# Kernel optimization log

Hardware: AMD Instinct MI355X
Metric: run time of the kernel (lower is better)

## Reference

```python
import jax, jax.numpy as jnp
import numpy as np

N_NODES = 70839  # num_user + num_item from config
N_EDGES = 2_000_000
EMB_DIM = 64
EPS = 1e-12  # torch F.normalize default eps


def setup_inputs() -> dict:
    key = jax.random.key(0)
    k1, k2, k3, k4 = jax.random.split(key, 4)
    ego_embedding = jax.random.normal(k1, (N_NODES, EMB_DIM), dtype=jnp.float32)
    edge_weight = jax.random.uniform(k2, (N_EDGES,), dtype=jnp.float32)
    edge_src = jax.random.randint(k3, (N_EDGES,), 0, N_NODES, dtype=jnp.int32)
    edge_dst = jax.random.randint(k4, (N_EDGES,), 0, N_NODES, dtype=jnp.int32)
    return {
        "ego_embedding": ego_embedding,
        "edge_weight": edge_weight,
        "edge_src": edge_src,
        "edge_dst": edge_dst,
    }


def reference(ego_embedding, edge_weight, edge_src, edge_dst):
    # message: m_e = h[src_e] * w_e   (u_mul_e)
    m = ego_embedding[edge_src] * edge_weight[:, None]          # [E, D]
    # reduce: h_v = sum_{e: dst_e = v} m_e   (fn.sum)
    h = jax.ops.segment_sum(m, edge_dst, num_segments=N_NODES)  # [N, D]
    # F.normalize(h, dim=1, p=2): x / max(||x||_2, eps)
    norm = jnp.linalg.norm(h, axis=1, keepdims=True)
    return h / jnp.maximum(norm, EPS)
```

## Files before the change

kernel.cpp:

```cpp
#include <hip/hip_runtime.h>
#include <hip/hip_fp16.h>

#define EMB_D 64
#define SB 1024
#define SPAN 128
#define MAXG 1024
#define NCHUNK2 512
#define CHMAX 4096
#define TILE 4096
#define CAST_BLOCKS 256


__device__ __forceinline__ float h15_to_float(unsigned int bits) {
    return __half2float(__ushort_as_half((unsigned short)bits));
}

__global__ void a1_cast_hist(const float2* __restrict__ embin,
                             __half2* __restrict__ emb16, int n2,
                             const int* __restrict__ dst,
                             int* __restrict__ cntT,
                             int E, int G, int chunk) {
    if (blockIdx.x < CAST_BLOCKS) {
        int i = blockIdx.x * blockDim.x + threadIdx.x;
        int st = CAST_BLOCKS * blockDim.x;
        for (; i < n2; i += st)
            emb16[i] = __float22half2_rn(embin[i]);
    } else {
        __shared__ int bins[MAXG];
        int hb = blockIdx.x - CAST_BLOCKS;
        for (int g = threadIdx.x; g < G; g += blockDim.x) bins[g] = 0;
        __syncthreads();
        int beg = hb * chunk;
        int end = min(beg + chunk, E);
        for (int i = beg + threadIdx.x; i < end; i += blockDim.x)
            atomicAdd(&bins[dst[i] >> 7], 1);
        __syncthreads();
        for (int g = threadIdx.x; g < G; g += blockDim.x)
            cntT[g * NCHUNK2 + hb] = bins[g];
    }
}

__global__ void scan_reduceB(const int* __restrict__ counts,
                             int* __restrict__ partial, int M) {
    __shared__ int wsum[16];
    const int tid = threadIdx.x, lane = tid & 63, wid = tid >> 6;
    int i = blockIdx.x * SB + tid;
    int v = (i < M) ? counts[i] : 0;
    #pragma unroll
    for (int off = 32; off > 0; off >>= 1)
        v += __shfl_xor(v, off, 64);
    if (lane == 0) wsum[wid] = v;
    __syncthreads();
    if (tid == 0) {
        int s = 0;
        #pragma unroll
        for (int k = 0; k < 16; ++k) s += wsum[k];
        partial[blockIdx.x] = s;
    }
}

__global__ void scan_partials(const int* __restrict__ partial,
                              int* __restrict__ blockoff,
                              int* __restrict__ offsets, int numB, int M) {
    __shared__ int wsum[16];
    __shared__ int wpre[16];
    __shared__ int carry;
    const int tid = threadIdx.x, lane = tid & 63, wid = tid >> 6;
    if (tid == 0) carry = 0;
    const int nPass = (numB + SB - 1) / SB;
    for (int p = 0; p < nPass; ++p) {
        __syncthreads();
        int base = carry;
        int idx = p * SB + tid;
        int v = (idx < numB) ? partial[idx] : 0;
        int x = v;
        #pragma unroll
        for (int off = 1; off < 64; off <<= 1) {
            int t = __shfl_up(x, off, 64);
            if (lane >= off) x += t;
        }
        if (lane == 63) wsum[wid] = x;
        __syncthreads();
        if (wid == 0) {
            int s = (lane < 16) ? wsum[lane] : 0;
            #pragma unroll
            for (int off = 1; off < 16; off <<= 1) {
                int t = __shfl_up(s, off, 64);
                if (lane >= off) s += t;
            }
            if (lane < 16) wpre[lane] = s;
        }
        __syncthreads();
        int excl = base + ((wid > 0) ? wpre[wid - 1] : 0) + (x - v);
        if (idx < numB) blockoff[idx] = excl;
        __syncthreads();
        if (tid == 0) carry = base + wpre[15];
    }
    __syncthreads();
    if (tid == 0) offsets[M] = carry;
}

__global__ void scan_applyB(const int* __restrict__ counts,
                            const int* __restrict__ blockoff,
                            int* __restrict__ offsets, int M) {
    __shared__ int wsum[16];
    __shared__ int wpre[16];
    const int tid = threadIdx.x, lane = tid & 63, wid = tid >> 6;
    int i = blockIdx.x * SB + tid;
    int v = (i < M) ? counts[i] : 0;
    int x = v;
    #pragma unroll
    for (int off = 1; off < 64; off <<= 1) {
        int t = __shfl_up(x, off, 64);
        if (lane >= off) x += t;
    }
    if (lane == 63) wsum[wid] = x;
    __syncthreads();
    if (wid == 0) {
        int s = (lane < 16) ? wsum[lane] : 0;
        #pragma unroll
        for (int off = 1; off < 16; off <<= 1) {
            int t = __shfl_up(s, off, 64);
            if (lane >= off) s += t;
        }
        if (lane < 16) wpre[lane] = s;
    }
    __syncthreads();
    int excl = blockoff[blockIdx.x] + ((wid > 0) ? wpre[wid - 1] : 0) + (x - v);
    if (i < M) offsets[i] = excl;
}

__global__ __launch_bounds__(512) void partition_sort(
        const int* __restrict__ src,
        const int* __restrict__ dst,
        const float* __restrict__ w,
        const int* __restrict__ cntT,
        const int* __restrict__ scanT,
        uint2* __restrict__ stream8,
        int E, int G, int chunk) {
    __shared__ uint2 recs[CHMAX];
    __shared__ int cur[MAXG];
    __shared__ int delta[MAXG];
    __shared__ int wtot[8];

    const int tid = threadIdx.x, lane = tid & 63, wv = tid >> 6;
    const int b = blockIdx.x;
    const int beg = b * chunk;
    const int end = min(beg + chunk, E);
    const int n = end - beg;

    const int K = (G + 511) >> 9;
    int vals[2];
    int acc = 0;
    #pragma unroll
    for (int k = 0; k < 2; ++k) {
        int g = tid * K + k;
        int c = (k < K && g < G) ? cntT[g * NCHUNK2 + b] : 0;
        vals[k] = c;
        acc += c;
    }
    int x = acc;
    #pragma unroll
    for (int off = 1; off < 64; off <<= 1) {
        int t = __shfl_up(x, off, 64);
        if (lane >= off) x += t;
    }
    if (lane == 63) wtot[wv] = x;
    __syncthreads();
    int woff = 0;
    #pragma unroll
    for (int k2 = 0; k2 < 8; ++k2)
        woff += (k2 < wv) ? wtot[k2] : 0;
    int run = woff + x - acc;
    #pragma unroll
    for (int k = 0; k < 2; ++k) {
        int g = tid * K + k;
        if (k < K && g < G) {
            cur[g] = run;
            delta[g] = scanT[g * NCHUNK2 + b] - run;
            run += vals[k];
        }
    }
    __syncthreads();

    for (int i = beg + tid; i < end; i += 512) {
        int d = dst[i];
        unsigned int wb = __half_as_ushort(__float2half_rn(w[i]));
        unsigned int pk = ((unsigned int)src[i] << 15) | (wb & 0x7FFFu);
        int g = d >> 7;
        int j = atomicAdd(&cur[g], 1);
        recs[j] = make_uint2(pk, (unsigned int)(d & (SPAN - 1)) |
                                 ((unsigned int)g << 7));
    }
    __syncthreads();

    for (int j = tid; j < n; j += 512) {
        uint2 r = recs[j];
        int g = (int)(r.y >> 7);
        stream8[delta[g] + j] = make_uint2(r.x, r.y & (SPAN - 1u));
    }
}

__global__ __launch_bounds__(512) void gather_fused(
        const char* __restrict__ emb16b,
        const uint2* __restrict__ stream8,
        const int* __restrict__ scanT,
        float* __restrict__ out, int N) {
    __shared__ uint2 lrec[TILE];
    __shared__ unsigned int srt[TILE];
    __shared__ int hcnt[SPAN];
    __shared__ int nstart[SPAN];
    __shared__ int cur[SPAN];
    __shared__ int wtot[2];

    const int g = blockIdx.x;
    const int tid = threadIdx.x;
    const int lane = tid & 63, wv = tid >> 6;
    const int base = scanT[g * NCHUNK2];
    const int endE = scanT[(g + 1) * NCHUNK2];
    const int crew = tid >> 4;
    const int ql = tid & 15;
    const int sub = ql >> 3;
    const int sl = ql & 7;
    const unsigned qlo = (unsigned)(sl << 4);

    float4 accA[4], accB[4];
    #pragma unroll
    for (int ni = 0; ni < 4; ++ni) {
        accA[ni] = make_float4(0.f, 0.f, 0.f, 0.f);
        accB[ni] = make_float4(0.f, 0.f, 0.f, 0.f);
    }

    for (int tb = base; tb < endE; tb += TILE) {
        const int n = min(TILE, endE - tb);
        if (tid < SPAN) hcnt[tid] = 0;
        __syncthreads();
        for (int j = tid; j < n; j += 512) {
            uint2 r = stream8[tb + j];
            lrec[j] = r;
            atomicAdd(&hcnt[r.y], 1);
        }
        __syncthreads();
        int v = (tid < SPAN) ? hcnt[tid] : 0;
        int x = v;
        #pragma unroll
        for (int off = 1; off < 64; off <<= 1) {
            int t = __shfl_up(x, off, 64);
            if (lane >= off) x += t;
        }
        if (wv < 2 && lane == 63) wtot[wv] = x;
        __syncthreads();
        if (tid < SPAN) {
            int excl = x - v + ((wv == 1) ? wtot[0] : 0);
            nstart[tid] = excl;
            cur[tid] = excl;
        }
        __syncthreads();
        for (int j = tid; j < n; j += 512) {
            uint2 r = lrec[j];
            int slot = atomicAdd(&cur[r.y], 1);
            srt[slot] = r.x;
        }
        __syncthreads();
        #pragma unroll
        for (int ni = 0; ni < 4; ++ni) {
            int nd = crew + (ni << 5);
            int s = nstart[nd];
            int e = cur[nd];
            float4 aA = accA[ni];
            float4 aB = accB[ni];
            int k0 = s + sub;
            unsigned int pk0 = (k0 < e) ? srt[k0] : 0u;
            uint4 r0 = *reinterpret_cast<const uint4*>(
                emb16b + ((pk0 >> 15) * 128u + qlo));
            for (int k = k0; k < e; k += 2) {
                int k1 = k + 2;
                unsigned int pk1 = (k1 < e) ? srt[k1] : 0u;
                uint4 r1 = *reinterpret_cast<const uint4*>(
                    emb16b + ((pk1 >> 15) * 128u + qlo));
                float wt = h15_to_float(pk0 & 0x7FFFu);
                float2 x01 = __half22float2(*reinterpret_cast<__half2*>(&r0.x));
                float2 x23 = __half22float2(*reinterpret_cast<__half2*>(&r0.y));
                float2 x45 = __half22float2(*reinterpret_cast<__half2*>(&r0.z));
                float2 x67 = __half22float2(*reinterpret_cast<__half2*>(&r0.w));
                aA.x = fmaf(x01.x, wt, aA.x);
                aA.y = fmaf(x01.y, wt, aA.y);
                aA.z = fmaf(x23.x, wt, aA.z);
                aA.w = fmaf(x23.y, wt, aA.w);
                aB.x = fmaf(x45.x, wt, aB.x);
                aB.y = fmaf(x45.y, wt, aB.y);
                aB.z = fmaf(x67.x, wt, aB.z);
                aB.w = fmaf(x67.y, wt, aB.w);
                pk0 = pk1; r0 = r1;
            }
            accA[ni] = aA;
            accB[ni] = aB;
        }
        __syncthreads();
    }

    #pragma unroll
    for (int ni = 0; ni < 4; ++ni) {
        accA[ni].x += __shfl_xor(accA[ni].x, 8, 64);
        accA[ni].y += __shfl_xor(accA[ni].y, 8, 64);
        accA[ni].z += __shfl_xor(accA[ni].z, 8, 64);
        accA[ni].w += __shfl_xor(accA[ni].w, 8, 64);
        accB[ni].x += __shfl_xor(accB[ni].x, 8, 64);
        accB[ni].y += __shfl_xor(accB[ni].y, 8, 64);
        accB[ni].z += __shfl_xor(accB[ni].z, 8, 64);
        accB[ni].w += __shfl_xor(accB[ni].w, 8, 64);
        int node = g * SPAN + crew + (ni << 5);
        float4 aA = accA[ni];
        float4 aB = accB[ni];
        float ss = aA.x * aA.x + aA.y * aA.y + aA.z * aA.z + aA.w * aA.w
                 + aB.x * aB.x + aB.y * aB.y + aB.z * aB.z + aB.w * aB.w;
        ss += __shfl_xor(ss, 1, 64);
        ss += __shfl_xor(ss, 2, 64);
        ss += __shfl_xor(ss, 4, 64);
        float scale = 1.0f / fmaxf(sqrtf(ss), 1e-12f);
        if (node < N) {
            float4 a = sub ? aB : aA;
            float4 o = make_float4(a.x * scale, a.y * scale,
                                   a.z * scale, a.w * scale);
            *reinterpret_cast<float4*>(out + (size_t)node * EMB_D
                                       + (sl << 3) + (sub << 2)) = o;
        }
    }
}

__global__ void group_csr2(const uint2* __restrict__ stream8,
                           const int* __restrict__ scanT,
                           unsigned int* __restrict__ packed,
                           int* __restrict__ offsets, int N, int E) {
    __shared__ int hcnt[SPAN];
    __shared__ int cur[SPAN];
    __shared__ int wtot[4];
    int g = blockIdx.x;
    int tid = threadIdx.x;
    int base = scanT[g * NCHUNK2];
    int endE = scanT[(g + 1) * NCHUNK2];
    if (tid < SPAN) hcnt[tid] = 0;
    __syncthreads();
    for (int i = base + tid; i < endE; i += blockDim.x)
        atomicAdd(&hcnt[stream8[i].y], 1);
    __syncthreads();
    int v = (tid < SPAN) ? hcnt[tid] : 0;
    int lane = tid & 63, wv = tid >> 6;
    int x = v;
    #pragma unroll
    for (int off = 1; off < 64; off <<= 1) {
        int t = __shfl_up(x, off, 64);
        if (lane >= off) x += t;
    }
    if (lane == 63) wtot[wv] = x;
    __syncthreads();
    if (tid < SPAN) {
        int excl = x - v + ((wv == 1) ? wtot[0] : 0);
        cur[tid] = base + excl;
        int node = g * SPAN + tid;
        if (node < N) offsets[node] = base + excl;
    }
    if (g == 0 && tid == 0) offsets[N] = E;
    __syncthreads();
    for (int i = base + tid; i < endE; i += blockDim.x) {
        uint2 r = stream8[i];
        int slot = atomicAdd(&cur[r.y], 1);
        packed[slot] = r.x;
    }
}

__global__ __launch_bounds__(256) void gatherV_kernel(
        const char* __restrict__ emb16b,
        const int* __restrict__ offsets,
        const unsigned int* __restrict__ packed,
        float* __restrict__ out, int N) {
    int node = blockIdx.x * 4 + (threadIdx.x >> 6);
    int lane = threadIdx.x & 63;
    if (node >= N) return;
    int q  = lane >> 3;
    int ql = lane & 7;
    const unsigned qlo = (unsigned)(ql << 4);

    int beg = offsets[node];
    int end = offsets[node + 1];

    float a0=0.f,a1=0.f,a2=0.f,a3=0.f,a4=0.f,a5=0.f,a6=0.f,a7=0.f;

    int idx0 = beg + q;
    int idx1 = idx0 + 8;
    int idx2 = idx1 + 8;
    unsigned int pk0 = (idx0 < end) ? packed[idx0] : 0u;
    unsigned int pk1 = (idx1 < end) ? packed[idx1] : 0u;
    unsigned int pk2 = (idx2 < end) ? packed[idx2] : 0u;
    uint4 r0 = *reinterpret_cast<const uint4*>(emb16b + ((pk0 >> 15) * 128u + qlo));
    uint4 r1 = *reinterpret_cast<const uint4*>(emb16b + ((pk1 >> 15) * 128u + qlo));

    for (int j = beg; j < end; j += 8) {
        uint4 r2 = *reinterpret_cast<const uint4*>(
            emb16b + ((pk2 >> 15) * 128u + qlo));
        int idx3 = idx2 + 8;
        unsigned int pk3 = (idx3 < end) ? packed[idx3] : 0u;

        float wt = h15_to_float(pk0 & 0x7FFFu);
        float2 x01 = __half22float2(*reinterpret_cast<__half2*>(&r0.x));
        float2 x23 = __half22float2(*reinterpret_cast<__half2*>(&r0.y));
        float2 x45 = __half22float2(*reinterpret_cast<__half2*>(&r0.z));
        float2 x67 = __half22float2(*reinterpret_cast<__half2*>(&r0.w));
        a0 = fmaf(x01.x, wt, a0);
        a1 = fmaf(x01.y, wt, a1);
        a2 = fmaf(x23.x, wt, a2);
        a3 = fmaf(x23.y, wt, a3);
        a4 = fmaf(x45.x, wt, a4);
        a5 = fmaf(x45.y, wt, a5);
        a6 = fmaf(x67.x, wt, a6);
        a7 = fmaf(x67.y, wt, a7);

        pk0 = pk1; pk1 = pk2; pk2 = pk3;
        r0 = r1; r1 = r2;
        idx2 = idx3;
    }

    #pragma unroll
    for (int off = 8; off < 64; off <<= 1) {
        a0 += __shfl_xor(a0, off, 64);
        a1 += __shfl_xor(a1, off, 64);
        a2 += __shfl_xor(a2, off, 64);
        a3 += __shfl_xor(a3, off, 64);
        a4 += __shfl_xor(a4, off, 64);
        a5 += __shfl_xor(a5, off, 64);
        a6 += __shfl_xor(a6, off, 64);
        a7 += __shfl_xor(a7, off, 64);
    }
    float ss = a0*a0 + a1*a1 + a2*a2 + a3*a3 + a4*a4 + a5*a5 + a6*a6 + a7*a7;
    ss += __shfl_xor(ss, 1, 64);
    ss += __shfl_xor(ss, 2, 64);
    ss += __shfl_xor(ss, 4, 64);
    float scale = 1.0f / fmaxf(sqrtf(ss), 1e-12f);

    if (q == 0) {
        float4* po = reinterpret_cast<float4*>(out + (size_t)node * EMB_D
                                               + (ql << 3));
        po[0] = make_float4(a0 * scale, a1 * scale, a2 * scale, a3 * scale);
        po[1] = make_float4(a4 * scale, a5 * scale, a6 * scale, a7 * scale);
    }
}

__global__ void lightgcn_scatter(const float* __restrict__ emb,
                                 const float* __restrict__ w,
                                 const int* __restrict__ src,
                                 const int* __restrict__ dst,
                                 float* __restrict__ h, int E) {
    long long t = (long long)blockIdx.x * blockDim.x + threadIdx.x;
    int e = (int)(t >> 4);
    int d = (int)(t & 15) << 2;
    if (e >= E) return;
    int s = src[e]; int v = dst[e]; float wt = w[e];
    const float4 m = *reinterpret_cast<const float4*>(emb + (size_t)s * EMB_D + d);
    float* o = h + (size_t)v * EMB_D + d;
    unsafeAtomicAdd(o + 0, m.x * wt);
    unsafeAtomicAdd(o + 1, m.y * wt);
    unsafeAtomicAdd(o + 2, m.z * wt);
    unsafeAtomicAdd(o + 3, m.w * wt);
}

__global__ void lightgcn_normalize(float* __restrict__ h, int N) {
    int row = blockIdx.x * (blockDim.x >> 6) + (threadIdx.x >> 6);
    int lane = threadIdx.x & 63;
    if (row >= N) return;
    float x = h[(size_t)row * EMB_D + lane];
    float ss = x * x;
    #pragma unroll
    for (int off = 32; off > 0; off >>= 1)
        ss += __shfl_xor(ss, off, 64);
    h[(size_t)row * EMB_D + lane] = x / fmaxf(sqrtf(ss), 1e-12f);
}

extern "C" void kernel_launch(void* const* d_in, const int* in_sizes, int n_in,
                              void* d_out, int out_size, void* d_ws, size_t ws_size,
                              hipStream_t stream) {
    const float* emb = (const float*)d_in[0];
    const float* w   = (const float*)d_in[1];
    const int*   src = (const int*)d_in[2];
    const int*   dst = (const int*)d_in[3];
    float* out = (float*)d_out;

    const int N = in_sizes[0] / EMB_D;
    const int E = in_sizes[1];
    const int block = 256;
    const int G = (N + SPAN - 1) / SPAN;

    const int M3 = G * NCHUNK2;
    const int numB3 = (M3 + SB - 1) / SB;
    const int chunk3 = (E + NCHUNK2 - 1) / NCHUNK2;

    size_t intsA5 = (size_t)M3 + (size_t)(M3 + 1) + 2 * (size_t)numB3;
    size_t strOff5 = (intsA5 * sizeof(int) + 15) & ~(size_t)15;
    size_t embOff5 = (strOff5 + (size_t)E * sizeof(uint2) + 15) & ~(size_t)15;
    size_t neededA5 = embOff5 + (size_t)N * EMB_D * sizeof(__half);

    size_t intsA3 = (size_t)M3 + (size_t)(M3 + 1) + 2 * (size_t)numB3
                  + (size_t)(N + 1);
    size_t strOff = (intsA3 * sizeof(int) + 15) & ~(size_t)15;
    size_t pkdOff = strOff + (size_t)E * sizeof(uint2);
    size_t embOff3 = (pkdOff + (size_t)E * sizeof(unsigned int) + 15)
                     & ~(size_t)15;
    size_t neededA3 = embOff3 + (size_t)N * EMB_D * sizeof(__half);

    if (ws_size >= neededA5 && G <= MAXG && chunk3 <= CHMAX &&
        E < (1 << 28) && N < (1 << 17)) {
        int* cntT     = (int*)d_ws;
        int* scanT    = cntT + M3;
        int* partial  = scanT + M3 + 1;
        int* blockoff = partial + numB3;
        uint2* stream8 = (uint2*)((char*)d_ws + strOff5);
        __half2* emb16 = (__half2*)((char*)d_ws + embOff5);

        int n2 = N * (EMB_D / 2);

        a1_cast_hist<<<CAST_BLOCKS + NCHUNK2, block, 0, stream>>>(
            (const float2*)emb, emb16, n2, dst, cntT, E, G, chunk3);

        scan_reduceB<<<numB3, SB, 0, stream>>>(cntT, partial, M3);
        scan_partials<<<1, SB, 0, stream>>>(partial, blockoff, scanT, numB3, M3);
        scan_applyB<<<numB3, SB, 0, stream>>>(cntT, blockoff, scanT, M3);

        partition_sort<<<NCHUNK2, 512, 0, stream>>>(src, dst, w, cntT, scanT,
                                                    stream8, E, G, chunk3);

        gather_fused<<<G, 512, 0, stream>>>((const char*)emb16, stream8,
                                            scanT, out, N);
    } else if (ws_size >= neededA3 && G <= MAXG && chunk3 <= CHMAX &&
               E < (1 << 28) && N < (1 << 17)) {
        int* cntT     = (int*)d_ws;
        int* scanT    = cntT + M3;
        int* partial  = scanT + M3 + 1;
        int* blockoff = partial + numB3;
        int* offsets  = blockoff + numB3;
        uint2* stream8 = (uint2*)((char*)d_ws + strOff);
        unsigned int* packed = (unsigned int*)((char*)d_ws + pkdOff);
        __half2* emb16 = (__half2*)((char*)d_ws + embOff3);

        int n2 = N * (EMB_D / 2);

        a1_cast_hist<<<CAST_BLOCKS + NCHUNK2, block, 0, stream>>>(
            (const float2*)emb, emb16, n2, dst, cntT, E, G, chunk3);

        scan_reduceB<<<numB3, SB, 0, stream>>>(cntT, partial, M3);
        scan_partials<<<1, SB, 0, stream>>>(partial, blockoff, scanT, numB3, M3);
        scan_applyB<<<numB3, SB, 0, stream>>>(cntT, blockoff, scanT, M3);

        partition_sort<<<NCHUNK2, 512, 0, stream>>>(src, dst, w, cntT, scanT,
                                                    stream8, E, G, chunk3);
        group_csr2<<<G, block, 0, stream>>>(stream8, scanT, packed, offsets,
                                            N, E);

        int gridN = (N + 3) / 4;
        gatherV_kernel<<<gridN, 256, 0, stream>>>((const char*)emb16, offsets,
                                                  packed, out, N);
    } else {
        hipMemsetAsync(d_out, 0, (size_t)out_size * sizeof(float), stream);
        long long total = (long long)E * 16;
        int grid = (int)((total + block - 1) / block);
        lightgcn_scatter<<<grid, block, 0, stream>>>(emb, w, src, dst, out, E);
        int gridN = (N + 3) / 4;
        lightgcn_normalize<<<gridN, 256, 0, stream>>>(out, N);
    }
}
```

Baseline: 175.4 us.

## Sort edges by destination group and source slice for gather locality

Changes the partition key from the destination group alone to the destination group combined with a 16K-node source slice. Within each destination group, edges then arrive ordered by source range, so gathers of half-precision embedding rows should hit cache better. The scan now runs in place on the count table, which drops the separate scan buffer, and the unused CSR fallback path is removed. The cost is a histogram and scan over three to five times more bins (about 2800 keys times 512 chunks) and larger shared-memory tables in the sort kernel.

```diff
diff --git a/kernel.cpp b/kernel.cpp
--- a/kernel.cpp
+++ b/kernel.cpp
@@ -5,14 +5,44 @@
 #define SB 1024
 #define SPAN 128
 #define MAXG 1024
+#define MAXK 3072
 #define NCHUNK2 512
 #define CHMAX 4096
 #define TILE 4096
+#define SLICE_SH 14
 #define CAST_BLOCKS 256
 
 
 __device__ __forceinline__ float h15_to_float(unsigned int bits) {
     return __half2float(__ushort_as_half((unsigned short)bits));
+}
+
+__global__ void a1_cast_histK(const float2* __restrict__ embin,
+                              __half2* __restrict__ emb16, int n2,
+                              const int* __restrict__ src,
+                              const int* __restrict__ dst,
+                              int* __restrict__ cntT,
+                              int E, int NK, int S, int chunk) {
+    if (blockIdx.x < CAST_BLOCKS) {
+        int i = blockIdx.x * blockDim.x + threadIdx.x;
+        int st = CAST_BLOCKS * blockDim.x;
+        for (; i < n2; i += st)
+            emb16[i] = __float22half2_rn(embin[i]);
+    } else {
+        __shared__ int bins[MAXK];
+        int hb = blockIdx.x - CAST_BLOCKS;
+        for (int k = threadIdx.x; k < NK; k += blockDim.x) bins[k] = 0;
+        __syncthreads();
+        int beg = hb * chunk;
+        int end = min(beg + chunk, E);
+        for (int i = beg + threadIdx.x; i < end; i += blockDim.x) {
+            int key = (dst[i] >> 7) * S + (src[i] >> SLICE_SH);
+            atomicAdd(&bins[key], 1);
+        }
+        __syncthreads();
+        for (int k = threadIdx.x; k < NK; k += blockDim.x)
+            cntT[k * NCHUNK2 + hb] = bins[k];
+    }
 }
 
 __global__ void a1_cast_hist(const float2* __restrict__ embin,
@@ -130,6 +160,110 @@
     if (i < M) offsets[i] = excl;
 }
 
+__global__ void scan_apply_ip(int* __restrict__ data,
+                              const int* __restrict__ blockoff, int M) {
+    __shared__ int wsum[16];
+    __shared__ int wpre[16];
+    const int tid = threadIdx.x, lane = tid & 63, wid = tid >> 6;
+    int i = blockIdx.x * SB + tid;
+    int v = (i < M) ? data[i] : 0;
+    int x = v;
+    #pragma unroll
+    for (int off = 1; off < 64; off <<= 1) {
+        int t = __shfl_up(x, off, 64);
+        if (lane >= off) x += t;
+    }
+    if (lane == 63) wsum[wid] = x;
+    __syncthreads();
+    if (wid == 0) {
+        int s = (lane < 16) ? wsum[lane] : 0;
+        #pragma unroll
+        for (int off = 1; off < 16; off <<= 1) {
+            int t = __shfl_up(s, off, 64);
+            if (lane >= off) s += t;
+        }
+        if (lane < 16) wpre[lane] = s;
+    }
+    __syncthreads();
+    int excl = blockoff[blockIdx.x] + ((wid > 0) ? wpre[wid - 1] : 0) + (x - v);
+    if (i < M) data[i] = excl;
+}
+
+__global__ __launch_bounds__(512) void partition_sortK(
+        const int* __restrict__ src,
+        const int* __restrict__ dst,
+        const float* __restrict__ w,
+        const int* __restrict__ scanT,
+        uint2* __restrict__ stream8,
+        int E, int NK, int S, int chunk) {
+    __shared__ uint2 recs[CHMAX];
+    __shared__ int cur[MAXK];
+    __shared__ int delta[MAXK];
+    __shared__ int wtot[8];
+
+    const int tid = threadIdx.x, lane = tid & 63, wv = tid >> 6;
+    const int b = blockIdx.x;
+    const int beg = b * chunk;
+    const int end = min(beg + chunk, E);
+    const int n = end - beg;
+
+    const int K = (NK + 511) >> 9;
+    int vals[6], bases[6];
+    int acc = 0;
+    #pragma unroll
+    for (int k = 0; k < 6; ++k) {
+        int key = tid * K + k;
+        int c = 0, bs = 0;
+        if (k < K && key < NK) {
+            bs = scanT[key * NCHUNK2 + b];
+            c = scanT[key * NCHUNK2 + b + 1] - bs;
+        }
+        vals[k] = c;
+        bases[k] = bs;
+        acc += c;
+    }
+    int x = acc;
+    #pragma unroll
+    for (int off = 1; off < 64; off <<= 1) {
+        int t = __shfl_up(x, off, 64);
+        if (lane >= off) x += t;
+    }
+    if (lane == 63) wtot[wv] = x;
+    __syncthreads();
+    int woff = 0;
+    #pragma unroll
+    for (int k2 = 0; k2 < 8; ++k2)
+        woff += (k2 < wv) ? wtot[k2] : 0;
+    int run = woff + x - acc;
+    #pragma unroll
+    for (int k = 0; k < 6; ++k) {
+        int key = tid * K + k;
+        if (k < K && key < NK) {
+            cur[key] = run;
+            delta[key] = bases[k] - run;
+            run += vals[k];
+        }
+    }
+    __syncthreads();
+
+    for (int i = beg + tid; i < end; i += 512) {
+        int d = dst[i];
+        int key = (d >> 7) * S + (src[i] >> SLICE_SH);
+        unsigned int wb = __half_as_ushort(__float2half_rn(w[i]));
+        unsigned int pk = ((unsigned int)src[i] << 15) | (wb & 0x7FFFu);
+        int j = atomicAdd(&cur[key], 1);
+        recs[j] = make_uint2(pk, (unsigned int)(d & (SPAN - 1)) |
+                                 ((unsigned int)key << 7));
+    }
+    __syncthreads();
+
+    for (int j = tid; j < n; j += 512) {
+        uint2 r = recs[j];
+        int key = (int)(r.y >> 7);
+        stream8[delta[key] + j] = make_uint2(r.x, r.y & (SPAN - 1u));
+    }
+}
+
 __global__ __launch_bounds__(512) void partition_sort(
         const int* __restrict__ src,
         const int* __restrict__ dst,
@@ -205,7 +339,7 @@
         const char* __restrict__ emb16b,
         const uint2* __restrict__ stream8,
         const int* __restrict__ scanT,
-        float* __restrict__ out, int N) {
+        float* __restrict__ out, int N, int SN) {
     __shared__ uint2 lrec[TILE];
     __shared__ unsigned int srt[TILE];
     __shared__ int hcnt[SPAN];
@@ -216,8 +350,8 @@
     const int g = blockIdx.x;
     const int tid = threadIdx.x;
     const int lane = tid & 63, wv = tid >> 6;
-    const int base = scanT[g * NCHUNK2];
-    const int endE = scanT[(g + 1) * NCHUNK2];
+    const int base = scanT[(size_t)g * SN];
+    const int endE = scanT[(size_t)(g + 1) * SN];
     const int crew = tid >> 4;
     const int ql = tid & 15;
     const int sub = ql >> 3;
@@ -328,123 +462,6 @@
     }
 }
 
-__global__ void group_csr2(const uint2* __restrict__ stream8,
-                           const int* __restrict__ scanT,
-                           unsigned int* __restrict__ packed,
-                           int* __restrict__ offsets, int N, int E) {
-    __shared__ int hcnt[SPAN];
-    __shared__ int cur[SPAN];
-    __shared__ int wtot[4];
-    int g = blockIdx.x;
-    int tid = threadIdx.x;
-    int base = scanT[g * NCHUNK2];
-    int endE = scanT[(g + 1) * NCHUNK2];
-    if (tid < SPAN) hcnt[tid] = 0;
-    __syncthreads();
-    for (int i = base + tid; i < endE; i += blockDim.x)
-        atomicAdd(&hcnt[stream8[i].y], 1);
-    __syncthreads();
-    int v = (tid < SPAN) ? hcnt[tid] : 0;
-    int lane = tid & 63, wv = tid >> 6;
-    int x = v;
-    #pragma unroll
-    for (int off = 1; off < 64; off <<= 1) {
-        int t = __shfl_up(x, off, 64);
-        if (lane >= off) x += t;
-    }
-    if (lane == 63) wtot[wv] = x;
-    __syncthreads();
-    if (tid < SPAN) {
-        int excl = x - v + ((wv == 1) ? wtot[0] : 0);
-        cur[tid] = base + excl;
-        int node = g * SPAN + tid;
-        if (node < N) offsets[node] = base + excl;
-    }
-    if (g == 0 && tid == 0) offsets[N] = E;
-    __syncthreads();
-    for (int i = base + tid; i < endE; i += blockDim.x) {
-        uint2 r = stream8[i];
-        int slot = atomicAdd(&cur[r.y], 1);
-        packed[slot] = r.x;
-    }
-}
-
-__global__ __launch_bounds__(256) void gatherV_kernel(
-        const char* __restrict__ emb16b,
-        const int* __restrict__ offsets,
-        const unsigned int* __restrict__ packed,
-        float* __restrict__ out, int N) {
-    int node = blockIdx.x * 4 + (threadIdx.x >> 6);
-    int lane = threadIdx.x & 63;
-    if (node >= N) return;
-    int q  = lane >> 3;
-    int ql = lane & 7;
-    const unsigned qlo = (unsigned)(ql << 4);
-
-    int beg = offsets[node];
-    int end = offsets[node + 1];
-
-    float a0=0.f,a1=0.f,a2=0.f,a3=0.f,a4=0.f,a5=0.f,a6=0.f,a7=0.f;
-
-    int idx0 = beg + q;
-    int idx1 = idx0 + 8;
-    int idx2 = idx1 + 8;
-    unsigned int pk0 = (idx0 < end) ? packed[idx0] : 0u;
-    unsigned int pk1 = (idx1 < end) ? packed[idx1] : 0u;
-    unsigned int pk2 = (idx2 < end) ? packed[idx2] : 0u;
-    uint4 r0 = *reinterpret_cast<const uint4*>(emb16b + ((pk0 >> 15) * 128u + qlo));
-    uint4 r1 = *reinterpret_cast<const uint4*>(emb16b + ((pk1 >> 15) * 128u + qlo));
-
-    for (int j = beg; j < end; j += 8) {
-        uint4 r2 = *reinterpret_cast<const uint4*>(
-            emb16b + ((pk2 >> 15) * 128u + qlo));
-        int idx3 = idx2 + 8;
-        unsigned int pk3 = (idx3 < end) ? packed[idx3] : 0u;
-
-        float wt = h15_to_float(pk0 & 0x7FFFu);
-        float2 x01 = __half22float2(*reinterpret_cast<__half2*>(&r0.x));
-        float2 x23 = __half22float2(*reinterpret_cast<__half2*>(&r0.y));
-        float2 x45 = __half22float2(*reinterpret_cast<__half2*>(&r0.z));
-        float2 x67 = __half22float2(*reinterpret_cast<__half2*>(&r0.w));
-        a0 = fmaf(x01.x, wt, a0);
-        a1 = fmaf(x01.y, wt, a1);
-        a2 = fmaf(x23.x, wt, a2);
-        a3 = fmaf(x23.y, wt, a3);
-        a4 = fmaf(x45.x, wt, a4);
-        a5 = fmaf(x45.y, wt, a5);
-        a6 = fmaf(x67.x, wt, a6);
-        a7 = fmaf(x67.y, wt, a7);
-
-        pk0 = pk1; pk1 = pk2; pk2 = pk3;
-        r0 = r1; r1 = r2;
-        idx2 = idx3;
-    }
-
-    #pragma unroll
-    for (int off = 8; off < 64; off <<= 1) {
-        a0 += __shfl_xor(a0, off, 64);
-        a1 += __shfl_xor(a1, off, 64);
-        a2 += __shfl_xor(a2, off, 64);
-        a3 += __shfl_xor(a3, off, 64);
-        a4 += __shfl_xor(a4, off, 64);
-        a5 += __shfl_xor(a5, off, 64);
-        a6 += __shfl_xor(a6, off, 64);
-        a7 += __shfl_xor(a7, off, 64);
-    }
-    float ss = a0*a0 + a1*a1 + a2*a2 + a3*a3 + a4*a4 + a5*a5 + a6*a6 + a7*a7;
-    ss += __shfl_xor(ss, 1, 64);
-    ss += __shfl_xor(ss, 2, 64);
-    ss += __shfl_xor(ss, 4, 64);
-    float scale = 1.0f / fmaxf(sqrtf(ss), 1e-12f);
-
-    if (q == 0) {
-        float4* po = reinterpret_cast<float4*>(out + (size_t)node * EMB_D
-                                               + (ql << 3));
-        po[0] = make_float4(a0 * scale, a1 * scale, a2 * scale, a3 * scale);
-        po[1] = make_float4(a4 * scale, a5 * scale, a6 * scale, a7 * scale);
-    }
-}
-
 __global__ void lightgcn_scatter(const float* __restrict__ emb,
                                  const float* __restrict__ w,
                                  const int* __restrict__ src,
@@ -489,25 +506,49 @@
     const int block = 256;
     const int G = (N + SPAN - 1) / SPAN;
 
+    const int S4 = (N + (1 << SLICE_SH) - 1) >> SLICE_SH;
+    const int NK4 = G * S4;
+    const int M4 = NK4 * NCHUNK2;
+    const int numB4 = (M4 + SB - 1) / SB;
+    const int chunk4 = (E + NCHUNK2 - 1) / NCHUNK2;
+    const int SN4 = S4 * NCHUNK2;
+    size_t intsA7 = (size_t)(M4 + 1) + 2 * (size_t)numB4;
+    size_t strOff7 = (intsA7 * sizeof(int) + 15) & ~(size_t)15;
+    size_t embOff7 = (strOff7 + (size_t)E * sizeof(uint2) + 15) & ~(size_t)15;
+    size_t neededA7 = embOff7 + (size_t)N * EMB_D * sizeof(__half);
+
     const int M3 = G * NCHUNK2;
     const int numB3 = (M3 + SB - 1) / SB;
     const int chunk3 = (E + NCHUNK2 - 1) / NCHUNK2;
-
     size_t intsA5 = (size_t)M3 + (size_t)(M3 + 1) + 2 * (size_t)numB3;
     size_t strOff5 = (intsA5 * sizeof(int) + 15) & ~(size_t)15;
     size_t embOff5 = (strOff5 + (size_t)E * sizeof(uint2) + 15) & ~(size_t)15;
     size_t neededA5 = embOff5 + (size_t)N * EMB_D * sizeof(__half);
 
-    size_t intsA3 = (size_t)M3 + (size_t)(M3 + 1) + 2 * (size_t)numB3
-                  + (size_t)(N + 1);
-    size_t strOff = (intsA3 * sizeof(int) + 15) & ~(size_t)15;
-    size_t pkdOff = strOff + (size_t)E * sizeof(uint2);
-    size_t embOff3 = (pkdOff + (size_t)E * sizeof(unsigned int) + 15)
-                     & ~(size_t)15;
-    size_t neededA3 = embOff3 + (size_t)N * EMB_D * sizeof(__half);
-
-    if (ws_size >= neededA5 && G <= MAXG && chunk3 <= CHMAX &&
+    if (ws_size >= neededA7 && NK4 <= MAXK && chunk4 <= CHMAX &&
         E < (1 << 28) && N < (1 << 17)) {
+        int* cntT     = (int*)d_ws;
+        int* partial  = cntT + M4 + 1;
+        int* blockoff = partial + numB4;
+        uint2* stream8 = (uint2*)((char*)d_ws + strOff7);
+        __half2* emb16 = (__half2*)((char*)d_ws + embOff7);
+
+        int n2 = N * (EMB_D / 2);
+
+        a1_cast_histK<<<CAST_BLOCKS + NCHUNK2, block, 0, stream>>>(
+            (const float2*)emb, emb16, n2, src, dst, cntT, E, NK4, S4, chunk4);
+
+        scan_reduceB<<<numB4, SB, 0, stream>>>(cntT, partial, M4);
+        scan_partials<<<1, SB, 0, stream>>>(partial, blockoff, cntT, numB4, M4);
+        scan_apply_ip<<<numB4, SB, 0, stream>>>(cntT, blockoff, M4);
+
+        partition_sortK<<<NCHUNK2, 512, 0, stream>>>(src, dst, w, cntT,
+                                                     stream8, E, NK4, S4,
+                                                     chunk4);
+        gather_fused<<<G, 512, 0, stream>>>((const char*)emb16, stream8, cntT,
+                                            out, N, SN4);
+    } else if (ws_size >= neededA5 && G <= MAXG && chunk3 <= CHMAX &&
+               E < (1 << 28) && N < (1 << 17)) {
         int* cntT     = (int*)d_ws;
         int* scanT    = cntT + M3;
         int* partial  = scanT + M3 + 1;
@@ -528,35 +569,7 @@
                                                     stream8, E, G, chunk3);
 
         gather_fused<<<G, 512, 0, stream>>>((const char*)emb16, stream8,
-                                            scanT, out, N);
-    } else if (ws_size >= neededA3 && G <= MAXG && chunk3 <= CHMAX &&
-               E < (1 << 28) && N < (1 << 17)) {
-        int* cntT     = (int*)d_ws;
-        int* scanT    = cntT + M3;
-        int* partial  = scanT + M3 + 1;
-        int* blockoff = partial + numB3;
-        int* offsets  = blockoff + numB3;
-        uint2* stream8 = (uint2*)((char*)d_ws + strOff);
-        unsigned int* packed = (unsigned int*)((char*)d_ws + pkdOff);
-        __half2* emb16 = (__half2*)((char*)d_ws + embOff3);
-
-        int n2 = N * (EMB_D / 2);
-
-        a1_cast_hist<<<CAST_BLOCKS + NCHUNK2, block, 0, stream>>>(
-            (const float2*)emb, emb16, n2, dst, cntT, E, G, chunk3);
-
-        scan_reduceB<<<numB3, SB, 0, stream>>>(cntT, partial, M3);
-        scan_partials<<<1, SB, 0, stream>>>(partial, blockoff, scanT, numB3, M3);
-        scan_applyB<<<numB3, SB, 0, stream>>>(cntT, blockoff, scanT, M3);
-
-        partition_sort<<<NCHUNK2, 512, 0, stream>>>(src, dst, w, cntT, scanT,
-                                                    stream8, E, G, chunk3);
-        group_csr2<<<G, block, 0, stream>>>(stream8, scanT, packed, offsets,
-                                            N, E);
-
-        int gridN = (N + 3) / 4;
-        gatherV_kernel<<<gridN, 256, 0, stream>>>((const char*)emb16, offsets,
-                                                  packed, out, N);
+                                            scanT, out, N, NCHUNK2);
     } else {
         hipMemsetAsync(d_out, 0, (size_t)out_size * sizeof(float), stream);
         long long total = (long long)E * 16;
```

Measured after the change: 205.2 us. 17.0% more time.

## Halve node-group span to 64, merge scan kernels, and slim fused gather

Applied to the files above, without the earlier changes.

Nodes are now bucketed into groups of 64 instead of 128, which doubles the number of gather blocks and halves per-block accumulator state. The gather kernel drops its shared-memory record copy and instead re-reads the edge stream from global memory, shrinking LDS use so more blocks can fit per CU. The single-block partial scan and the apply pass are merged into one kernel in which every block reduces all partials itself, removing a launch. The fp32-to-fp16 cast is widened to float4 loads, and the unused CSR fallback path is deleted. In exchange the histogram and partition stages handle more bins, and each gather tile reads the stream twice from global memory.

```diff
diff --git a/kernel.cpp b/kernel.cpp
--- a/kernel.cpp
+++ b/kernel.cpp
@@ -3,11 +3,12 @@
 
 #define EMB_D 64
 #define SB 1024
-#define SPAN 128
-#define MAXG 1024
+#define SPAN 64
+#define SPAN_SH 6
+#define MAXG 2048
 #define NCHUNK2 512
 #define CHMAX 4096
-#define TILE 4096
+#define TILE2 2048
 #define CAST_BLOCKS 256
 
 
@@ -15,16 +16,37 @@
     return __half2float(__ushort_as_half((unsigned short)bits));
 }
 
-__global__ void a1_cast_hist(const float2* __restrict__ embin,
-                             __half2* __restrict__ emb16, int n2,
+__device__ __forceinline__ uint4 rowld(const char* base, unsigned int pk,
+                                       unsigned int qlo) {
+    return *reinterpret_cast<const uint4*>(base + ((pk >> 15) * 128u + qlo));
+}
+
+__device__ __forceinline__ void fma8(float4& a, float4& b, uint4 r, float wt) {
+    float2 x01 = __half22float2(*reinterpret_cast<__half2*>(&r.x));
+    float2 x23 = __half22float2(*reinterpret_cast<__half2*>(&r.y));
+    float2 x45 = __half22float2(*reinterpret_cast<__half2*>(&r.z));
+    float2 x67 = __half22float2(*reinterpret_cast<__half2*>(&r.w));
+    a.x = fmaf(x01.x, wt, a.x); a.y = fmaf(x01.y, wt, a.y);
+    a.z = fmaf(x23.x, wt, a.z); a.w = fmaf(x23.y, wt, a.w);
+    b.x = fmaf(x45.x, wt, b.x); b.y = fmaf(x45.y, wt, b.y);
+    b.z = fmaf(x67.x, wt, b.z); b.w = fmaf(x67.y, wt, b.w);
+}
+
+__global__ void a1_cast_hist(const float4* __restrict__ embin,
+                             uint2* __restrict__ emb16, int n4,
                              const int* __restrict__ dst,
                              int* __restrict__ cntT,
                              int E, int G, int chunk) {
     if (blockIdx.x < CAST_BLOCKS) {
         int i = blockIdx.x * blockDim.x + threadIdx.x;
         int st = CAST_BLOCKS * blockDim.x;
-        for (; i < n2; i += st)
-            emb16[i] = __float22half2_rn(embin[i]);
+        for (; i < n4; i += st) {
+            float4 v = embin[i];
+            __half2 h0 = __float22half2_rn(make_float2(v.x, v.y));
+            __half2 h1 = __float22half2_rn(make_float2(v.z, v.w));
+            emb16[i] = make_uint2(*reinterpret_cast<unsigned int*>(&h0),
+                                  *reinterpret_cast<unsigned int*>(&h1));
+        }
     } else {
         __shared__ int bins[MAXG];
         int hb = blockIdx.x - CAST_BLOCKS;
@@ -33,7 +55,7 @@
         int beg = hb * chunk;
         int end = min(beg + chunk, E);
         for (int i = beg + threadIdx.x; i < end; i += blockDim.x)
-            atomicAdd(&bins[dst[i] >> 7], 1);
+            atomicAdd(&bins[dst[i] >> SPAN_SH], 1);
         __syncthreads();
         for (int g = threadIdx.x; g < G; g += blockDim.x)
             cntT[g * NCHUNK2 + hb] = bins[g];
@@ -59,54 +81,38 @@
     }
 }
 
-__global__ void scan_partials(const int* __restrict__ partial,
-                              int* __restrict__ blockoff,
-                              int* __restrict__ offsets, int numB, int M) {
+__global__ void scan_apply2(const int* __restrict__ counts,
+                            const int* __restrict__ partial,
+                            int* __restrict__ offsets, int M, int numB) {
+    __shared__ int wsA[16];
+    __shared__ int wsB[16];
     __shared__ int wsum[16];
     __shared__ int wpre[16];
-    __shared__ int carry;
+    __shared__ int s_boff;
     const int tid = threadIdx.x, lane = tid & 63, wid = tid >> 6;
-    if (tid == 0) carry = 0;
-    const int nPass = (numB + SB - 1) / SB;
-    for (int p = 0; p < nPass; ++p) {
-        __syncthreads();
-        int base = carry;
-        int idx = p * SB + tid;
-        int v = (idx < numB) ? partial[idx] : 0;
-        int x = v;
+    const int bid = blockIdx.x;
+
+    int pall = (tid < numB) ? partial[tid] : 0;
+    int ppre = (tid < bid) ? pall : 0;
+    int sa = pall, sb = ppre;
+    #pragma unroll
+    for (int off = 32; off > 0; off >>= 1) {
+        sa += __shfl_xor(sa, off, 64);
+        sb += __shfl_xor(sb, off, 64);
+    }
+    if (lane == 0) { wsA[wid] = sa; wsB[wid] = sb; }
+    __syncthreads();
+    if (tid == 0) {
+        int a = 0, b = 0;
         #pragma unroll
-        for (int off = 1; off < 64; off <<= 1) {
-            int t = __shfl_up(x, off, 64);
-            if (lane >= off) x += t;
-        }
-        if (lane == 63) wsum[wid] = x;
-        __syncthreads();
-        if (wid == 0) {
-            int s = (lane < 16) ? wsum[lane] : 0;
-            #pragma unroll
-            for (int off = 1; off < 16; off <<= 1) {
-                int t = __shfl_up(s, off, 64);
-                if (lane >= off) s += t;
-            }
-            if (lane < 16) wpre[lane] = s;
-        }
-        __syncthreads();
-        int excl = base + ((wid > 0) ? wpre[wid - 1] : 0) + (x - v);
-        if (idx < numB) blockoff[idx] = excl;
-        __syncthreads();
-        if (tid == 0) carry = base + wpre[15];
-    }
-    __syncthreads();
-    if (tid == 0) offsets[M] = carry;
-}
-
-__global__ void scan_applyB(const int* __restrict__ counts,
-                            const int* __restrict__ blockoff,
-                            int* __restrict__ offsets, int M) {
-    __shared__ int wsum[16];
-    __shared__ int wpre[16];
-    const int tid = threadIdx.x, lane = tid & 63, wid = tid >> 6;
-    int i = blockIdx.x * SB + tid;
+        for (int k = 0; k < 16; ++k) { a += wsA[k]; b += wsB[k]; }
+        s_boff = b;
+        if (bid == 0) offsets[M] = a;
+    }
+    __syncthreads();
+    const int boff = s_boff;
+
+    int i = bid * SB + tid;
     int v = (i < M) ? counts[i] : 0;
     int x = v;
     #pragma unroll
@@ -126,7 +132,7 @@
         if (lane < 16) wpre[lane] = s;
     }
     __syncthreads();
-    int excl = blockoff[blockIdx.x] + ((wid > 0) ? wpre[wid - 1] : 0) + (x - v);
+    int excl = boff + ((wid > 0) ? wpre[wid - 1] : 0) + (x - v);
     if (i < M) offsets[i] = excl;
 }
 
@@ -150,10 +156,10 @@
     const int n = end - beg;
 
     const int K = (G + 511) >> 9;
-    int vals[2];
+    int vals[4];
     int acc = 0;
     #pragma unroll
-    for (int k = 0; k < 2; ++k) {
+    for (int k = 0; k < 4; ++k) {
         int g = tid * K + k;
         int c = (k < K && g < G) ? cntT[g * NCHUNK2 + b] : 0;
         vals[k] = c;
@@ -173,7 +179,7 @@
         woff += (k2 < wv) ? wtot[k2] : 0;
     int run = woff + x - acc;
     #pragma unroll
-    for (int k = 0; k < 2; ++k) {
+    for (int k = 0; k < 4; ++k) {
         int g = tid * K + k;
         if (k < K && g < G) {
             cur[g] = run;
@@ -187,35 +193,32 @@
         int d = dst[i];
         unsigned int wb = __half_as_ushort(__float2half_rn(w[i]));
         unsigned int pk = ((unsigned int)src[i] << 15) | (wb & 0x7FFFu);
-        int g = d >> 7;
+        int g = d >> SPAN_SH;
         int j = atomicAdd(&cur[g], 1);
         recs[j] = make_uint2(pk, (unsigned int)(d & (SPAN - 1)) |
-                                 ((unsigned int)g << 7));
+                                 ((unsigned int)g << SPAN_SH));
     }
     __syncthreads();
 
     for (int j = tid; j < n; j += 512) {
         uint2 r = recs[j];
-        int g = (int)(r.y >> 7);
+        int g = (int)(r.y >> SPAN_SH);
         stream8[delta[g] + j] = make_uint2(r.x, r.y & (SPAN - 1u));
     }
 }
 
-__global__ __launch_bounds__(512) void gather_fused(
+__global__ __launch_bounds__(512) void gather_fused64(
         const char* __restrict__ emb16b,
         const uint2* __restrict__ stream8,
         const int* __restrict__ scanT,
         float* __restrict__ out, int N) {
-    __shared__ uint2 lrec[TILE];
-    __shared__ unsigned int srt[TILE];
+    __shared__ unsigned int srt[TILE2];
     __shared__ int hcnt[SPAN];
     __shared__ int nstart[SPAN];
     __shared__ int cur[SPAN];
-    __shared__ int wtot[2];
 
     const int g = blockIdx.x;
     const int tid = threadIdx.x;
-    const int lane = tid & 63, wv = tid >> 6;
     const int base = scanT[g * NCHUNK2];
     const int endE = scanT[(g + 1) * NCHUNK2];
     const int crew = tid >> 4;
@@ -224,46 +227,40 @@
     const int sl = ql & 7;
     const unsigned qlo = (unsigned)(sl << 4);
 
-    float4 accA[4], accB[4];
-    #pragma unroll
-    for (int ni = 0; ni < 4; ++ni) {
+    float4 accA[2], accB[2];
+    #pragma unroll
+    for (int ni = 0; ni < 2; ++ni) {
         accA[ni] = make_float4(0.f, 0.f, 0.f, 0.f);
         accB[ni] = make_float4(0.f, 0.f, 0.f, 0.f);
     }
 
-    for (int tb = base; tb < endE; tb += TILE) {
-        const int n = min(TILE, endE - tb);
+    for (int tb = base; tb < endE; tb += TILE2) {
+        const int n = min(TILE2, endE - tb);
         if (tid < SPAN) hcnt[tid] = 0;
+        __syncthreads();
+        for (int j = tid; j < n; j += 512)
+            atomicAdd(&hcnt[(int)stream8[tb + j].y], 1);
+        __syncthreads();
+        if (tid < SPAN) {
+            int v = hcnt[tid];
+            int x = v;
+            #pragma unroll
+            for (int off = 1; off < 64; off <<= 1) {
+                int t = __shfl_up(x, off, 64);
+                if (tid >= off) x += t;
+            }
+            nstart[tid] = x - v;
+            cur[tid] = x - v;
+        }
         __syncthreads();
         for (int j = tid; j < n; j += 512) {
             uint2 r = stream8[tb + j];
-            lrec[j] = r;
-            atomicAdd(&hcnt[r.y], 1);
-        }
-        __syncthreads();
-        int v = (tid < SPAN) ? hcnt[tid] : 0;
-        int x = v;
+            int slot = atomicAdd(&cur[(int)r.y], 1);
+            srt[slot] = r.x;
+        }
+        __syncthreads();
         #pragma unroll
-        for (int off = 1; off < 64; off <<= 1) {
-            int t = __shfl_up(x, off, 64);
-            if (lane >= off) x += t;
-        }
-        if (wv < 2 && lane == 63) wtot[wv] = x;
-        __syncthreads();
-        if (tid < SPAN) {
-            int excl = x - v + ((wv == 1) ? wtot[0] : 0);
-            nstart[tid] = excl;
-            cur[tid] = excl;
-        }
-        __syncthreads();
-        for (int j = tid; j < n; j += 512) {
-            uint2 r = lrec[j];
-            int slot = atomicAdd(&cur[r.y], 1);
-            srt[slot] = r.x;
-        }
-        __syncthreads();
-        #pragma unroll
-        for (int ni = 0; ni < 4; ++ni) {
+        for (int ni = 0; ni < 2; ++ni) {
             int nd = crew + (ni << 5);
             int s = nstart[nd];
             int e = cur[nd];
@@ -271,26 +268,12 @@
             float4 aB = accB[ni];
             int k0 = s + sub;
             unsigned int pk0 = (k0 < e) ? srt[k0] : 0u;
-            uint4 r0 = *reinterpret_cast<const uint4*>(
-                emb16b + ((pk0 >> 15) * 128u + qlo));
+            uint4 r0 = rowld(emb16b, pk0, qlo);
             for (int k = k0; k < e; k += 2) {
                 int k1 = k + 2;
                 unsigned int pk1 = (k1 < e) ? srt[k1] : 0u;
-                uint4 r1 = *reinterpret_cast<const uint4*>(
-                    emb16b + ((pk1 >> 15) * 128u + qlo));
-                float wt = h15_to_float(pk0 & 0x7FFFu);
-                float2 x01 = __half22float2(*reinterpret_cast<__half2*>(&r0.x));
-                float2 x23 = __half22float2(*reinterpret_cast<__half2*>(&r0.y));
-                float2 x45 = __half22float2(*reinterpret_cast<__half2*>(&r0.z));
-                float2 x67 = __half22float2(*reinterpret_cast<__half2*>(&r0.w));
-                aA.x = fmaf(x01.x, wt, aA.x);
-                aA.y = fmaf(x01.y, wt, aA.y);
-                aA.z = fmaf(x23.x, wt, aA.z);
-                aA.w = fmaf(x23.y, wt, aA.w);
-                aB.x = fmaf(x45.x, wt, aB.x);
-                aB.y = fmaf(x45.y, wt, aB.y);
-                aB.z = fmaf(x67.x, wt, aB.z);
-                aB.w = fmaf(x67.y, wt, aB.w);
+                uint4 r1 = rowld(emb16b, pk1, qlo);
+                fma8(aA, aB, r0, h15_to_float(pk0 & 0x7FFFu));
                 pk0 = pk1; r0 = r1;
             }
             accA[ni] = aA;
@@ -300,7 +283,7 @@
     }
 
     #pragma unroll
-    for (int ni = 0; ni < 4; ++ni) {
+    for (int ni = 0; ni < 2; ++ni) {
         accA[ni].x += __shfl_xor(accA[ni].x, 8, 64);
         accA[ni].y += __shfl_xor(accA[ni].y, 8, 64);
         accA[ni].z += __shfl_xor(accA[ni].z, 8, 64);
@@ -328,123 +311,6 @@
     }
 }
 
-__global__ void group_csr2(const uint2* __restrict__ stream8,
-                           const int* __restrict__ scanT,
-                           unsigned int* __restrict__ packed,
-                           int* __restrict__ offsets, int N, int E) {
-    __shared__ int hcnt[SPAN];
-    __shared__ int cur[SPAN];
-    __shared__ int wtot[4];
-    int g = blockIdx.x;
-    int tid = threadIdx.x;
-    int base = scanT[g * NCHUNK2];
-    int endE = scanT[(g + 1) * NCHUNK2];
-    if (tid < SPAN) hcnt[tid] = 0;
-    __syncthreads();
-    for (int i = base + tid; i < endE; i += blockDim.x)
-        atomicAdd(&hcnt[stream8[i].y], 1);
-    __syncthreads();
-    int v = (tid < SPAN) ? hcnt[tid] : 0;
-    int lane = tid & 63, wv = tid >> 6;
-    int x = v;
-    #pragma unroll
-    for (int off = 1; off < 64; off <<= 1) {
-        int t = __shfl_up(x, off, 64);
-        if (lane >= off) x += t;
-    }
-    if (lane == 63) wtot[wv] = x;
-    __syncthreads();
-    if (tid < SPAN) {
-        int excl = x - v + ((wv == 1) ? wtot[0] : 0);
-        cur[tid] = base + excl;
-        int node = g * SPAN + tid;
-        if (node < N) offsets[node] = base + excl;
-    }
-    if (g == 0 && tid == 0) offsets[N] = E;
-    __syncthreads();
-    for (int i = base + tid; i < endE; i += blockDim.x) {
-        uint2 r = stream8[i];
-        int slot = atomicAdd(&cur[r.y], 1);
-        packed[slot] = r.x;
-    }
-}
-
-__global__ __launch_bounds__(256) void gatherV_kernel(
-        const char* __restrict__ emb16b,
-        const int* __restrict__ offsets,
-        const unsigned int* __restrict__ packed,
-        float* __restrict__ out, int N) {
-    int node = blockIdx.x * 4 + (threadIdx.x >> 6);
-    int lane = threadIdx.x & 63;
-    if (node >= N) return;
-    int q  = lane >> 3;
-    int ql = lane & 7;
-    const unsigned qlo = (unsigned)(ql << 4);
-
-    int beg = offsets[node];
-    int end = offsets[node + 1];
-
-    float a0=0.f,a1=0.f,a2=0.f,a3=0.f,a4=0.f,a5=0.f,a6=0.f,a7=0.f;
-
-    int idx0 = beg + q;
-    int idx1 = idx0 + 8;
-    int idx2 = idx1 + 8;
-    unsigned int pk0 = (idx0 < end) ? packed[idx0] : 0u;
-    unsigned int pk1 = (idx1 < end) ? packed[idx1] : 0u;
-    unsigned int pk2 = (idx2 < end) ? packed[idx2] : 0u;
-    uint4 r0 = *reinterpret_cast<const uint4*>(emb16b + ((pk0 >> 15) * 128u + qlo));
-    uint4 r1 = *reinterpret_cast<const uint4*>(emb16b + ((pk1 >> 15) * 128u + qlo));
-
-    for (int j = beg; j < end; j += 8) {
-        uint4 r2 = *reinterpret_cast<const uint4*>(
-            emb16b + ((pk2 >> 15) * 128u + qlo));
-        int idx3 = idx2 + 8;
-        unsigned int pk3 = (idx3 < end) ? packed[idx3] : 0u;
-
-        float wt = h15_to_float(pk0 & 0x7FFFu);
-        float2 x01 = __half22float2(*reinterpret_cast<__half2*>(&r0.x));
-        float2 x23 = __half22float2(*reinterpret_cast<__half2*>(&r0.y));
-        float2 x45 = __half22float2(*reinterpret_cast<__half2*>(&r0.z));
-        float2 x67 = __half22float2(*reinterpret_cast<__half2*>(&r0.w));
-        a0 = fmaf(x01.x, wt, a0);
-        a1 = fmaf(x01.y, wt, a1);
-        a2 = fmaf(x23.x, wt, a2);
-        a3 = fmaf(x23.y, wt, a3);
-        a4 = fmaf(x45.x, wt, a4);
-        a5 = fmaf(x45.y, wt, a5);
-        a6 = fmaf(x67.x, wt, a6);
-        a7 = fmaf(x67.y, wt, a7);
-
-        pk0 = pk1; pk1 = pk2; pk2 = pk3;
-        r0 = r1; r1 = r2;
-        idx2 = idx3;
-    }
-
-    #pragma unroll
-    for (int off = 8; off < 64; off <<= 1) {
-        a0 += __shfl_xor(a0, off, 64);
-        a1 += __shfl_xor(a1, off, 64);
-        a2 += __shfl_xor(a2, off, 64);
-        a3 += __shfl_xor(a3, off, 64);
-        a4 += __shfl_xor(a4, off, 64);
-        a5 += __shfl_xor(a5, off, 64);
-        a6 += __shfl_xor(a6, off, 64);
-        a7 += __shfl_xor(a7, off, 64);
-    }
-    float ss = a0*a0 + a1*a1 + a2*a2 + a3*a3 + a4*a4 + a5*a5 + a6*a6 + a7*a7;
-    ss += __shfl_xor(ss, 1, 64);
-    ss += __shfl_xor(ss, 2, 64);
-    ss += __shfl_xor(ss, 4, 64);
-    float scale = 1.0f / fmaxf(sqrtf(ss), 1e-12f);
-
-    if (q == 0) {
-        float4* po = reinterpret_cast<float4*>(out + (size_t)node * EMB_D
-                                               + (ql << 3));
-        po[0] = make_float4(a0 * scale, a1 * scale, a2 * scale, a3 * scale);
-        po[1] = make_float4(a4 * scale, a5 * scale, a6 * scale, a7 * scale);
-    }
-}
-
 __global__ void lightgcn_scatter(const float* __restrict__ emb,
                                  const float* __restrict__ w,
                                  const int* __restrict__ src,
@@ -493,70 +359,32 @@
     const int numB3 = (M3 + SB - 1) / SB;
     const int chunk3 = (E + NCHUNK2 - 1) / NCHUNK2;
 
-    size_t intsA5 = (size_t)M3 + (size_t)(M3 + 1) + 2 * (size_t)numB3;
-    size_t strOff5 = (intsA5 * sizeof(int) + 15) & ~(size_t)15;
-    size_t embOff5 = (strOff5 + (size_t)E * sizeof(uint2) + 15) & ~(size_t)15;
-    size_t neededA5 = embOff5 + (size_t)N * EMB_D * sizeof(__half);
-
-    size_t intsA3 = (size_t)M3 + (size_t)(M3 + 1) + 2 * (size_t)numB3
-                  + (size_t)(N + 1);
-    size_t strOff = (intsA3 * sizeof(int) + 15) & ~(size_t)15;
-    size_t pkdOff = strOff + (size_t)E * sizeof(uint2);
-    size_t embOff3 = (pkdOff + (size_t)E * sizeof(unsigned int) + 15)
-                     & ~(size_t)15;
-    size_t neededA3 = embOff3 + (size_t)N * EMB_D * sizeof(__half);
-
-    if (ws_size >= neededA5 && G <= MAXG && chunk3 <= CHMAX &&
+    size_t intsA = (size_t)M3 + (size_t)(M3 + 1) + (size_t)numB3;
+    size_t strOff = (intsA * sizeof(int) + 15) & ~(size_t)15;
+    size_t embOff = (strOff + (size_t)E * sizeof(uint2) + 15) & ~(size_t)15;
+    size_t needed = embOff + (size_t)N * EMB_D * sizeof(__half);
+
+    if (ws_size >= needed && G <= MAXG && chunk3 <= CHMAX && numB3 <= SB &&
         E < (1 << 28) && N < (1 << 17)) {
         int* cntT     = (int*)d_ws;
         int* scanT    = cntT + M3;
         int* partial  = scanT + M3 + 1;
-        int* blockoff = partial + numB3;
-        uint2* stream8 = (uint2*)((char*)d_ws + strOff5);
-        __half2* emb16 = (__half2*)((char*)d_ws + embOff5);
-
-        int n2 = N * (EMB_D / 2);
+        uint2* stream8 = (uint2*)((char*)d_ws + strOff);
+        uint2* emb16 = (uint2*)((char*)d_ws + embOff);
+
+        int n4 = N * (EMB_D / 4);
 
         a1_cast_hist<<<CAST_BLOCKS + NCHUNK2, block, 0, stream>>>(
-            (const float2*)emb, emb16, n2, dst, cntT, E, G, chunk3);
+            (const float4*)emb, emb16, n4, dst, cntT, E, G, chunk3);
 
         scan_reduceB<<<numB3, SB, 0, stream>>>(cntT, partial, M3);
-        scan_partials<<<1, SB, 0, stream>>>(partial, blockoff, scanT, numB3, M3);
-        scan_applyB<<<numB3, SB, 0, stream>>>(cntT, blockoff, scanT, M3);
+        scan_apply2<<<numB3, SB, 0, stream>>>(cntT, partial, scanT, M3, numB3);
 
         partition_sort<<<NCHUNK2, 512, 0, stream>>>(src, dst, w, cntT, scanT,
                                                     stream8, E, G, chunk3);
 
-        gather_fused<<<G, 512, 0, stream>>>((const char*)emb16, stream8,
-                                            scanT, out, N);
-    } else if (ws_size >= neededA3 && G <= MAXG && chunk3 <= CHMAX &&
-               E < (1 << 28) && N < (1 << 17)) {
-        int* cntT     = (int*)d_ws;
-        int* scanT    = cntT + M3;
-        int* partial  = scanT + M3 + 1;
-        int* blockoff = partial + numB3;
-        int* offsets  = blockoff + numB3;
-        uint2* stream8 = (uint2*)((char*)d_ws + strOff);
-        unsigned int* packed = (unsigned int*)((char*)d_ws + pkdOff);
-        __half2* emb16 = (__half2*)((char*)d_ws + embOff3);
-
-        int n2 = N * (EMB_D / 2);
-
-        a1_cast_hist<<<CAST_BLOCKS + NCHUNK2, block, 0, stream>>>(
-            (const float2*)emb, emb16, n2, dst, cntT, E, G, chunk3);
-
-        scan_reduceB<<<numB3, SB, 0, stream>>>(cntT, partial, M3);
-        scan_partials<<<1, SB, 0, stream>>>(partial, blockoff, scanT, numB3, M3);
-        scan_applyB<<<numB3, SB, 0, stream>>>(cntT, blockoff, scanT, M3);
-
-        partition_sort<<<NCHUNK2, 512, 0, stream>>>(src, dst, w, cntT, scanT,
-                                                    stream8, E, G, chunk3);
-        group_csr2<<<G, block, 0, stream>>>(stream8, scanT, packed, offsets,
-                                            N, E);
-
-        int gridN = (N + 3) / 4;
-        gatherV_kernel<<<gridN, 256, 0, stream>>>((const char*)emb16, offsets,
-                                                  packed, out, N);
+        gather_fused64<<<G, 512, 0, stream>>>((const char*)emb16, stream8,
+                                              scanT, out, N);
     } else {
         hipMemsetAsync(d_out, 0, (size_t)out_size * sizeof(float), stream);
         long long total = (long long)E * 16;
```

New measurement: 187.3 us. 6.8% more time.
